# Performance work log

Measured on AMD Instinct MI355X. Metric: run time of the kernel, lower is better.

Reference implementation:

```python
import jax, jax.numpy as jnp
import numpy as np

NUM_HEADS = 16
HEAD_SIZE = 256
HIDDEN = NUM_HEADS * HEAD_SIZE  # 4096
ROTARY_DIM = 64
TOTAL_TOKENS = 8192
BATCH = 8
NUM_SLOTS = 16384


def setup_inputs() -> dict:
    key = jax.random.key(0)
    ks = jax.random.split(key, 6)
    hidden_states = jax.random.normal(ks[0], (TOTAL_TOKENS, HIDDEN), dtype=jnp.float32)
    w_qkv = jax.random.normal(ks[1], (3 * HIDDEN, HIDDEN), dtype=jnp.float32) * 0.02
    w_o = jax.random.normal(ks[2], (HIDDEN, HIDDEN), dtype=jnp.float32) * 0.02
    # cos/sin per token for the first rotary_dim dims (rotary_dim//2 freqs)
    cos = jax.random.uniform(ks[3], (TOTAL_TOKENS, ROTARY_DIM // 2), dtype=jnp.float32)
    sin = jax.random.uniform(ks[4], (TOTAL_TOKENS, ROTARY_DIM // 2), dtype=jnp.float32)
    key_cache = jnp.zeros((NUM_SLOTS, NUM_HEADS, HEAD_SIZE), dtype=jnp.float32)
    value_cache = jnp.zeros((NUM_SLOTS, NUM_HEADS, HEAD_SIZE), dtype=jnp.float32)
    slots = jnp.arange(TOTAL_TOKENS, dtype=jnp.int64) if jax.config.jax_enable_x64 else jnp.arange(TOTAL_TOKENS, dtype=jnp.int32)
    return {
        "hidden_states": hidden_states, "w_qkv": w_qkv, "w_o": w_o,
        "cos": cos, "sin": sin,
        "key_cache": key_cache, "value_cache": value_cache,
        "slots": slots, "batch_size": BATCH,
    }


def _apply_rope(x, cos, sin, rotary_dim):
    # x: [T, H, D]; rotate-half applied only to the first rotary_dim dims
    half = rotary_dim // 2
    x1 = x[..., :half]
    x2 = x[..., half:rotary_dim]
    c = cos[:, None, :]  # [T, 1, half]
    s = sin[:, None, :]
    rot = jnp.concatenate([x1 * c - x2 * s, x2 * c + x1 * s], axis=-1)
    return jnp.concatenate([rot, x[..., rotary_dim:]], axis=-1)


def reference(hidden_states, w_qkv, w_o, cos, sin, key_cache, value_cache, slots, batch_size):
    T, H = hidden_states.shape
    nh, hd = key_cache.shape[1], key_cache.shape[2]
    rotary_dim = 2 * cos.shape[1]
    scale = float(hd) ** -0.5

    # fused QKV projection (no bias), then split
    qkv = hidden_states @ w_qkv.T  # [T, 3H]
    q, k, v = jnp.split(qkv, 3, axis=1)
    q = q.reshape(T, nh, hd)
    k = k.reshape(T, nh, hd)
    v = v.reshape(T, nh, hd)

    # partial rotary embedding on first rotary_dim dims
    q = _apply_rope(q, cos, sin, rotary_dim)
    k = _apply_rope(k, cos, sin, rotary_dim)

    # KV-cache slot scatter, then gather back (prefill reads what was stored)
    key_cache = key_cache.at[slots].set(k)
    value_cache = value_cache.at[slots].set(v)
    k = key_cache[slots]
    v = value_cache[slots]

    # prefill flash-attention path: equal-length sequences, causal per sequence
    B = batch_size
    S = T // B
    qb = q.reshape(B, S, nh, hd)
    kb = k.reshape(B, S, nh, hd)
    vb = v.reshape(B, S, nh, hd)

    scores = jnp.einsum('bqhd,bkhd->bhqk', qb, kb) * scale  # [B, nh, S, S]
    causal = jnp.tril(jnp.ones((S, S), dtype=bool))
    scores = jnp.where(causal[None, None], scores, jnp.finfo(scores.dtype).min)
    attn = jax.nn.softmax(scores, axis=-1)
    out = jnp.einsum('bhqk,bkhd->bqhd', attn, vb).reshape(T, nh * hd)

    return out @ w_o.T
```

## Files before the change

### kernel.cpp

```cpp
#include <hip/hip_runtime.h>
#include <stdint.h>


typedef __bf16 bf16x8 __attribute__((ext_vector_type(8)));
typedef float f32x4 __attribute__((ext_vector_type(4)));

__device__ __forceinline__ unsigned short f2bf(float f) {
    union { float f; unsigned int u; } x;
    x.f = f;
    unsigned int r = x.u + 0x7fffu + ((x.u >> 16) & 1u);
    return (unsigned short)(r >> 16);
}

__device__ __forceinline__ float bf2f(unsigned short h) {
    union { unsigned int u; float f; } x;
    x.u = ((unsigned int)h) << 16;
    return x.f;
}

__device__ __forceinline__ void gld16(const void* g, void* l) {
    __builtin_amdgcn_global_load_lds(
        (const __attribute__((address_space(1))) void*)g,
        (__attribute__((address_space(3))) void*)l, 16, 0, 0);
}

__global__ __launch_bounds__(256) void cvt_bf16(const float* __restrict__ src,
                                                unsigned short* __restrict__ dst,
                                                long n4) {
    long i = (long)blockIdx.x * 256 + threadIdx.x;
    long stride = (long)gridDim.x * 256;
    for (; i < n4; i += stride) {
        float4 v = ((const float4*)src)[i];
        ushort4 o;
        o.x = f2bf(v.x); o.y = f2bf(v.y); o.z = f2bf(v.z); o.w = f2bf(v.w);
        ((ushort4*)dst)[i] = o;
    }
}

template <int EPI>
__global__ __launch_bounds__(512, 2) void gemm256(
    const unsigned short* __restrict__ A, long lda,
    const unsigned short* __restrict__ B, long ldb,
    int nkt, void* __restrict__ out,
    unsigned short* __restrict__ out2, unsigned short* __restrict__ out3) {
    __shared__ __attribute__((aligned(16))) unsigned short As[4 * 8192];
    __shared__ __attribute__((aligned(16))) unsigned short Bs[4 * 8192];

    const int tid = threadIdx.x;
    const int gx = gridDim.x;
    const int bid = blockIdx.y * gx + blockIdx.x;
    const int cpx = (gx * gridDim.y) >> 3;
    const int swz = (bid & 7) * cpx + (bid >> 3);
    const int ntile = swz % gx, mtile = swz / gx;

    const int l = tid & 63;
    const int wr = (tid >> 8) & 1, wc = (tid >> 6) & 3;
    const int lr = l & 15, lg = l >> 4;

    const int srow = tid >> 2;
    const int slc = (tid & 3) ^ ((tid >> 3) & 3);
    const unsigned short* Ag = A + (long)(mtile * 256 + srow) * lda + slc * 8;
    const unsigned short* Bg = B + (long)(ntile * 256 + srow) * ldb + slc * 8;
    unsigned short* lA = As + tid * 8;
    unsigned short* lB = Bs + tid * 8;

#define STAGE256(kt)                                              \
    {                                                             \
        const int s_ = (kt) & 3;                                  \
        const unsigned short* a_ = Ag + (long)(kt) * 32;          \
        const unsigned short* b_ = Bg + (long)(kt) * 32;          \
        gld16(a_, lA + s_ * 8192);                                \
        gld16(a_ + 128 * lda, lA + s_ * 8192 + 4096);             \
        gld16(b_, lB + s_ * 8192);                                \
        gld16(b_ + 128 * ldb, lB + s_ * 8192 + 4096);             \
    }

    int aoff[8], boff[4];
#pragma unroll
    for (int i = 0; i < 8; ++i) {
        const int r = wr * 128 + i * 16 + lr;
        aoff[i] = r * 32 + ((lg ^ ((r >> 1) & 3)) << 3);
    }
#pragma unroll
    for (int i = 0; i < 4; ++i) {
        const int r = wc * 64 + i * 16 + lr;
        boff[i] = r * 32 + ((lg ^ ((r >> 1) & 3)) << 3);
    }

    f32x4 acc[8][4];
#pragma unroll
    for (int i = 0; i < 8; ++i)
#pragma unroll
        for (int j = 0; j < 4; ++j) acc[i][j] = (f32x4)(0.0f);

    STAGE256(0);
    STAGE256(1);
    STAGE256(2);

    for (int t = 0; t < nkt; ++t) {
        if (t + 3 < nkt) {
            STAGE256(t + 3);
            asm volatile("s_waitcnt vmcnt(12)" ::: "memory");
        } else if (t + 2 < nkt) {
            asm volatile("s_waitcnt vmcnt(8)" ::: "memory");
        } else if (t + 1 < nkt) {
            asm volatile("s_waitcnt vmcnt(4)" ::: "memory");
        } else {
            asm volatile("s_waitcnt vmcnt(0)" ::: "memory");
        }
        __builtin_amdgcn_s_barrier();
        asm volatile("" ::: "memory");

        const unsigned short* as_ = As + ((t & 3) << 13);
        const unsigned short* bs_ = Bs + ((t & 3) << 13);
        bf16x8 af[8], bfr[4];
#pragma unroll
        for (int i = 0; i < 8; ++i) af[i] = *(const bf16x8*)(as_ + aoff[i]);
#pragma unroll
        for (int i = 0; i < 4; ++i) bfr[i] = *(const bf16x8*)(bs_ + boff[i]);

        __builtin_amdgcn_s_setprio(1);
#pragma unroll
        for (int mi = 0; mi < 8; ++mi)
#pragma unroll
            for (int ni = 0; ni < 4; ++ni)
                acc[mi][ni] = __builtin_amdgcn_mfma_f32_16x16x32_bf16(
                    af[mi], bfr[ni], acc[mi][ni], 0, 0, 0);
        __builtin_amdgcn_s_setprio(0);

        asm volatile("" ::: "memory");
        __builtin_amdgcn_s_barrier();
        asm volatile("" ::: "memory");
    }
#undef STAGE256

    const int mBase = mtile * 256 + wr * 128 + lg * 4;
    const int nBase = ntile * 256 + wc * 64 + lr;
#pragma unroll
    for (int mi = 0; mi < 8; ++mi) {
#pragma unroll
        for (int ni = 0; ni < 4; ++ni) {
#pragma unroll
            for (int r = 0; r < 4; ++r) {
                const int m = mBase + mi * 16 + r;
                const int n = nBase + ni * 16;
                const float v = acc[mi][ni][r];
                if (EPI == 0) {
                    const int which = n >> 12, h = (n >> 8) & 15, d = n & 255;
                    const int b = m >> 10, s = m & 1023;
                    const long idx = ((((long)b * 16 + h) << 10) + s) * 256 + d;
                    unsigned short* dst =
                        (which == 0) ? (unsigned short*)out : (which == 1 ? out2 : out3);
                    dst[idx] = f2bf(v);
                } else {
                    ((float*)out)[((long)m << 12) + n] = v;
                }
            }
        }
    }
}

template <int EPI>
__global__ __launch_bounds__(256) void gemm_bt(
    const unsigned short* __restrict__ A, long astride, long abatch,
    const unsigned short* __restrict__ B, long bstride, long bbatch,
    int kIters, void* __restrict__ out,
    unsigned short* __restrict__ out2, unsigned short* __restrict__ out3) {
    const int tid = threadIdx.x;
    const int ntile = blockIdx.x, mtile = blockIdx.y, bz = blockIdx.z;
    if (EPI == 1 && ntile > mtile) return;
    int kit = kIters;
    if (EPI == 2) kit = (mtile + 1) * 4;

    __shared__ __attribute__((aligned(16))) unsigned short As[128 * 32];
    __shared__ __attribute__((aligned(16))) unsigned short Bs[128 * 32];

    const unsigned short* Ab = A + (long)bz * abatch + (long)mtile * 128 * astride;
    const unsigned short* Bb = B + (long)bz * bbatch + (long)ntile * 128 * bstride;

    const int w = tid >> 6, l = tid & 63;
    const int wm = (w >> 1) * 64, wn = (w & 1) * 64;
    const int lr = l & 15;
    const int lc = l >> 4;

    const int c0 = tid, c1 = tid + 256;
    const int r0 = c0 >> 2, r1 = c1 >> 2;
    const int lc0 = (c0 & 3) ^ ((r0 >> 1) & 3);
    const int lc1 = (c1 & 3) ^ ((r1 >> 1) & 3);
    const long a0 = (long)r0 * astride + lc0 * 8;
    const long a1 = (long)r1 * astride + lc1 * 8;
    const long b0 = (long)r0 * bstride + lc0 * 8;
    const long b1 = (long)r1 * bstride + lc1 * 8;

    int aoff[4], boff[4];
#pragma unroll
    for (int i = 0; i < 4; ++i) {
        const int ra = wm + i * 16 + lr;
        aoff[i] = ra * 32 + ((lc ^ ((ra >> 1) & 3)) << 3);
        const int rb = wn + i * 16 + lr;
        boff[i] = rb * 32 + ((lc ^ ((rb >> 1) & 3)) << 3);
    }

    f32x4 acc[4][4];
#pragma unroll
    for (int i = 0; i < 4; ++i)
#pragma unroll
        for (int j = 0; j < 4; ++j) acc[i][j] = (f32x4)(0.0f);

    for (int kt = 0; kt < kit; ++kt) {
        const unsigned short* ak = Ab + kt * 32;
        const unsigned short* bk = Bb + kt * 32;
        __syncthreads();
        gld16(ak + a0, As + (long)c0 * 8);
        gld16(ak + a1, As + (long)c1 * 8);
        gld16(bk + b0, Bs + (long)c0 * 8);
        gld16(bk + b1, Bs + (long)c1 * 8);
        __syncthreads();

        bf16x8 af[4], bfv[4];
#pragma unroll
        for (int i = 0; i < 4; ++i) {
            af[i] = *(const bf16x8*)(As + aoff[i]);
            bfv[i] = *(const bf16x8*)(Bs + boff[i]);
        }
#pragma unroll
        for (int mi = 0; mi < 4; ++mi)
#pragma unroll
            for (int ni = 0; ni < 4; ++ni)
                acc[mi][ni] = __builtin_amdgcn_mfma_f32_16x16x32_bf16(
                    af[mi], bfv[ni], acc[mi][ni], 0, 0, 0);
    }

    const int mBase = mtile * 128 + wm + (l >> 4) * 4;
    const int nBase = ntile * 128 + wn + (l & 15);
#pragma unroll
    for (int mi = 0; mi < 4; ++mi) {
#pragma unroll
        for (int ni = 0; ni < 4; ++ni) {
#pragma unroll
            for (int r = 0; r < 4; ++r) {
                const int m = mBase + mi * 16 + r;
                const int n = nBase + ni * 16;
                const float v = acc[mi][ni][r];
                if (EPI == 1) {
                    ((float*)out)[((long)bz << 20) + ((long)m << 10) + n] = v * 0.0625f;
                } else if (EPI == 2) {
                    const int b = bz >> 4, h = bz & 15;
                    ((unsigned short*)out)[(((long)b << 10) + m) * 4096 + h * 256 + n] =
                        f2bf(v);
                }
            }
        }
    }
    (void)out2; (void)out3;
}

__global__ __launch_bounds__(256) void rope_qk(unsigned short* __restrict__ q_s,
                                               unsigned short* __restrict__ k_s,
                                               const float* __restrict__ cosp,
                                               const float* __restrict__ sinp) {
    const int tid = blockIdx.x * 256 + threadIdx.x;
    const int i = tid & 31;
    const int h = (tid >> 5) & 15;
    const int tok = tid >> 9;
    const int b = tok >> 10, s = tok & 1023;
    const long base = ((((long)b * 16 + h) << 10) + s) * 256 + i;
    const float c = cosp[tok * 32 + i];
    const float sn = sinp[tok * 32 + i];
    {
        float x1 = bf2f(q_s[base]), x2 = bf2f(q_s[base + 32]);
        q_s[base] = f2bf(x1 * c - x2 * sn);
        q_s[base + 32] = f2bf(x2 * c + x1 * sn);
    }
    {
        float x1 = bf2f(k_s[base]), x2 = bf2f(k_s[base + 32]);
        k_s[base] = f2bf(x1 * c - x2 * sn);
        k_s[base + 32] = f2bf(x2 * c + x1 * sn);
    }
}

__global__ __launch_bounds__(256) void vtrans(const unsigned short* __restrict__ v_s,
                                              unsigned short* __restrict__ vT) {
    __shared__ unsigned short tile[32][33];
    const int bh = blockIdx.z;
    const int s0 = blockIdx.x * 32, d0 = blockIdx.y * 32;
    const int x = threadIdx.x, y = threadIdx.y;
    const unsigned short* src = v_s + (((long)bh << 10) + s0) * 256 + d0;
#pragma unroll
    for (int j = 0; j < 4; ++j) tile[y * 4 + j][x] = src[(y * 4 + j) * 256 + x];
    __syncthreads();
    unsigned short* dst = vT + (((long)bh << 8) + d0) * 1024 + s0;
#pragma unroll
    for (int j = 0; j < 4; ++j) dst[(y * 4 + j) * 1024 + x] = tile[x][y * 4 + j];
}

__global__ __launch_bounds__(256) void softmax_rows(float* __restrict__ scores) {
    const int row = blockIdx.x;
    const int bh = row >> 10, q = row & 1023;
    float* srow = scores + ((long)bh << 20) + ((long)q << 10);
    const int t = threadIdx.x;

    float v[4];
#pragma unroll
    for (int j = 0; j < 4; ++j) {
        const int k = t + (j << 8);
        v[j] = (k <= q) ? srow[k] : -3.0e38f;
    }
    float mx = fmaxf(fmaxf(v[0], v[1]), fmaxf(v[2], v[3]));
#pragma unroll
    for (int off = 32; off >= 1; off >>= 1) mx = fmaxf(mx, __shfl_xor(mx, off));
    __shared__ float redmax[4];
    if ((t & 63) == 0) redmax[t >> 6] = mx;
    __syncthreads();
    mx = fmaxf(fmaxf(redmax[0], redmax[1]), fmaxf(redmax[2], redmax[3]));

    float p[4];
    float s = 0.0f;
#pragma unroll
    for (int j = 0; j < 4; ++j) {
        const int k = t + (j << 8);
        p[j] = (k <= q) ? __expf(v[j] - mx) : 0.0f;
        s += p[j];
    }
#pragma unroll
    for (int off = 32; off >= 1; off >>= 1) s += __shfl_xor(s, off);
    __shared__ float redsum[4];
    if ((t & 63) == 0) redsum[t >> 6] = s;
    __syncthreads();
    s = redsum[0] + redsum[1] + redsum[2] + redsum[3];
    const float inv = 1.0f / s;

    unsigned short* prow = (unsigned short*)srow;
    const int kend = (q & ~127) + 128;
#pragma unroll
    for (int j = 0; j < 4; ++j) {
        const int k = t + (j << 8);
        if (k < kend) prow[k] = f2bf(p[j] * inv);
    }
}

extern "C" void kernel_launch(void* const* d_in, const int* in_sizes, int n_in,
                              void* d_out, int out_size, void* d_ws, size_t ws_size,
                              hipStream_t stream) {
    const float* hidden = (const float*)d_in[0];
    const float* w_qkv  = (const float*)d_in[1];
    const float* w_o    = (const float*)d_in[2];
    const float* cosp   = (const float*)d_in[3];
    const float* sinp   = (const float*)d_in[4];

    const long SZ_WO = 33554432L, SZ_HEAD = 67108864L, SZ_SCORES = 536870912L;
    if (ws_size < (size_t)(SZ_WO + 5 * SZ_HEAD + SZ_SCORES)) return;
    char* p = (char*)d_ws;
    unsigned short* wo_b = (unsigned short*)p;  p += SZ_WO;
    unsigned short* q_s  = (unsigned short*)p;  p += SZ_HEAD;
    unsigned short* k_s  = (unsigned short*)p;  p += SZ_HEAD;
    unsigned short* v_s  = (unsigned short*)p;  p += SZ_HEAD;
    unsigned short* vT   = (unsigned short*)p;  p += SZ_HEAD;
    unsigned short* attn = (unsigned short*)p;  p += SZ_HEAD;
    char* X = p;
    unsigned short* hid_b  = (unsigned short*)X;
    unsigned short* wqkv_b = (unsigned short*)(X + SZ_HEAD);
    float* scores = (float*)X;

    cvt_bf16<<<8192, 256, 0, stream>>>(hidden, hid_b, (long)8192 * 4096 / 4);
    cvt_bf16<<<8192, 256, 0, stream>>>(w_qkv, wqkv_b, (long)12288 * 4096 / 4);
    cvt_bf16<<<4096, 256, 0, stream>>>(w_o, wo_b, (long)4096 * 4096 / 4);

    gemm256<0><<<dim3(48, 32, 1), 512, 0, stream>>>(
        hid_b, 4096, wqkv_b, 4096, 128, q_s, k_s, v_s);

    rope_qk<<<16384, 256, 0, stream>>>(q_s, k_s, cosp, sinp);

    vtrans<<<dim3(32, 8, 128), dim3(32, 8, 1), 0, stream>>>(v_s, vT);

    gemm_bt<1><<<dim3(8, 8, 128), 256, 0, stream>>>(
        q_s, 256, 262144, k_s, 256, 262144, 8, scores, nullptr, nullptr);

    softmax_rows<<<131072, 256, 0, stream>>>(scores);

    gemm_bt<2><<<dim3(2, 8, 128), 256, 0, stream>>>(
        (unsigned short*)scores, 2048, 2097152, vT, 1024, 262144, 0,
        attn, nullptr, nullptr);

    gemm256<1><<<dim3(16, 32, 1), 512, 0, stream>>>(
        attn, 4096, wo_b, 4096, 128, d_out, nullptr, nullptr);

    (void)in_sizes; (void)n_in; (void)out_size;
}
```

Measured before the change: 2.533 ms.

## Restructure 256x256 GEMM mainloop into four-phase ping-pong with split staging

```diff
diff --git a/kernel.cpp b/kernel.cpp
--- a/kernel.cpp
+++ b/kernel.cpp
@@ -38,13 +38,13 @@
 }
 
 template <int EPI>
-__global__ __launch_bounds__(512, 2) void gemm256(
+__global__ __launch_bounds__(512, 2) void gemm256p(
     const unsigned short* __restrict__ A, long lda,
     const unsigned short* __restrict__ B, long ldb,
     int nkt, void* __restrict__ out,
     unsigned short* __restrict__ out2, unsigned short* __restrict__ out3) {
-    __shared__ __attribute__((aligned(16))) unsigned short As[4 * 8192];
-    __shared__ __attribute__((aligned(16))) unsigned short Bs[4 * 8192];
+    __shared__ __attribute__((aligned(16))) unsigned short As[32768];
+    __shared__ __attribute__((aligned(16))) unsigned short Bs[32768];
 
     const int tid = threadIdx.x;
     const int gx = gridDim.x;
@@ -61,19 +61,33 @@
     const int slc = (tid & 3) ^ ((tid >> 3) & 3);
     const unsigned short* Ag = A + (long)(mtile * 256 + srow) * lda + slc * 8;
     const unsigned short* Bg = B + (long)(ntile * 256 + srow) * ldb + slc * 8;
-    unsigned short* lA = As + tid * 8;
-    unsigned short* lB = Bs + tid * 8;
-
-#define STAGE256(kt)                                              \
-    {                                                             \
-        const int s_ = (kt) & 3;                                  \
-        const unsigned short* a_ = Ag + (long)(kt) * 32;          \
-        const unsigned short* b_ = Bg + (long)(kt) * 32;          \
-        gld16(a_, lA + s_ * 8192);                                \
-        gld16(a_ + 128 * lda, lA + s_ * 8192 + 4096);             \
-        gld16(b_, lB + s_ * 8192);                                \
-        gld16(b_ + 128 * ldb, lB + s_ * 8192 + 4096);             \
-    }
+    unsigned short* lAs = As + tid * 8;
+    unsigned short* lBs = Bs + tid * 8;
+
+#define STAGE_A(t, kk)                                                 \
+    {                                                                  \
+        const unsigned short* g_ = Ag + (long)(t) * 64 + (kk) * 32;    \
+        unsigned short* d_ = lAs + (((t) & 1) * 16384 + (kk) * 8192);  \
+        gld16(g_, d_);                                                 \
+        gld16(g_ + 128 * lda, d_ + 4096);                              \
+    }
+#define STAGE_B(t, kk)                                                 \
+    {                                                                  \
+        const unsigned short* g_ = Bg + (long)(t) * 64 + (kk) * 32;    \
+        unsigned short* d_ = lBs + (((t) & 1) * 16384 + (kk) * 8192);  \
+        gld16(g_, d_);                                                 \
+        gld16(g_ + 128 * ldb, d_ + 4096);                              \
+    }
+#define WAITV(full_)                                                   \
+    if (full_) { asm volatile("s_waitcnt vmcnt(12)" ::: "memory"); }   \
+    else       { asm volatile("s_waitcnt vmcnt(0)" ::: "memory"); }
+#define LEADBAR()                                                      \
+    __builtin_amdgcn_s_barrier();                                      \
+    __builtin_amdgcn_sched_barrier(0)
+#define TRAILBAR()                                                     \
+    asm volatile("s_waitcnt lgkmcnt(0)" ::: "memory");                 \
+    __builtin_amdgcn_sched_barrier(0);                                 \
+    __builtin_amdgcn_s_barrier()
 
     int aoff[8], boff[4];
 #pragma unroll
@@ -93,46 +107,106 @@
 #pragma unroll
         for (int j = 0; j < 4; ++j) acc[i][j] = (f32x4)(0.0f);
 
-    STAGE256(0);
-    STAGE256(1);
-    STAGE256(2);
+    STAGE_A(0, 0); STAGE_B(0, 0); STAGE_A(0, 1); STAGE_B(0, 1);
+    STAGE_A(1, 0); STAGE_B(1, 0); STAGE_A(1, 1);
 
     for (int t = 0; t < nkt; ++t) {
-        if (t + 3 < nkt) {
-            STAGE256(t + 3);
-            asm volatile("s_waitcnt vmcnt(12)" ::: "memory");
-        } else if (t + 2 < nkt) {
-            asm volatile("s_waitcnt vmcnt(8)" ::: "memory");
-        } else if (t + 1 < nkt) {
-            asm volatile("s_waitcnt vmcnt(4)" ::: "memory");
-        } else {
-            asm volatile("s_waitcnt vmcnt(0)" ::: "memory");
-        }
-        __builtin_amdgcn_s_barrier();
-        asm volatile("" ::: "memory");
-
-        const unsigned short* as_ = As + ((t & 3) << 13);
-        const unsigned short* bs_ = Bs + ((t & 3) << 13);
-        bf16x8 af[8], bfr[4];
-#pragma unroll
-        for (int i = 0; i < 8; ++i) af[i] = *(const bf16x8*)(as_ + aoff[i]);
-#pragma unroll
-        for (int i = 0; i < 4; ++i) bfr[i] = *(const bf16x8*)(bs_ + boff[i]);
-
-        __builtin_amdgcn_s_setprio(1);
-#pragma unroll
-        for (int mi = 0; mi < 8; ++mi)
-#pragma unroll
-            for (int ni = 0; ni < 4; ++ni)
-                acc[mi][ni] = __builtin_amdgcn_mfma_f32_16x16x32_bf16(
-                    af[mi], bfr[ni], acc[mi][ni], 0, 0, 0);
-        __builtin_amdgcn_s_setprio(0);
-
-        asm volatile("" ::: "memory");
-        __builtin_amdgcn_s_barrier();
-        asm volatile("" ::: "memory");
-    }
-#undef STAGE256
+        const int p = t & 1;
+        const unsigned short* a0 = As + p * 16384;
+        const unsigned short* b0 = Bs + p * 16384;
+        const unsigned short* a1 = a0 + 8192;
+        const unsigned short* b1 = b0 + 8192;
+        const bool full = (t + 2 < nkt);
+
+        bf16x8 af[8];
+
+        if (t + 1 < nkt) STAGE_B(t + 1, 1);
+        WAITV(full);
+        LEADBAR();
+        {
+#pragma unroll
+            for (int mi = 0; mi < 8; ++mi)
+                af[mi] = *(const bf16x8*)(a0 + aoff[mi]);
+            bf16x8 f0 = *(const bf16x8*)(b0 + boff[0]);
+            bf16x8 f1 = *(const bf16x8*)(b0 + boff[1]);
+            __builtin_amdgcn_s_setprio(1);
+#pragma unroll
+            for (int mi = 0; mi < 8; ++mi)
+                acc[mi][0] = __builtin_amdgcn_mfma_f32_16x16x32_bf16(
+                    af[mi], f0, acc[mi][0], 0, 0, 0);
+#pragma unroll
+            for (int mi = 0; mi < 8; ++mi)
+                acc[mi][1] = __builtin_amdgcn_mfma_f32_16x16x32_bf16(
+                    af[mi], f1, acc[mi][1], 0, 0, 0);
+            __builtin_amdgcn_s_setprio(0);
+        }
+        TRAILBAR();
+
+        if (full) STAGE_A(t + 2, 0);
+        WAITV(full);
+        LEADBAR();
+        {
+            bf16x8 f2 = *(const bf16x8*)(b0 + boff[2]);
+            bf16x8 f3 = *(const bf16x8*)(b0 + boff[3]);
+            __builtin_amdgcn_s_setprio(1);
+#pragma unroll
+            for (int mi = 0; mi < 8; ++mi)
+                acc[mi][2] = __builtin_amdgcn_mfma_f32_16x16x32_bf16(
+                    af[mi], f2, acc[mi][2], 0, 0, 0);
+#pragma unroll
+            for (int mi = 0; mi < 8; ++mi)
+                acc[mi][3] = __builtin_amdgcn_mfma_f32_16x16x32_bf16(
+                    af[mi], f3, acc[mi][3], 0, 0, 0);
+            __builtin_amdgcn_s_setprio(0);
+        }
+        TRAILBAR();
+
+        if (full) STAGE_B(t + 2, 0);
+        WAITV(full);
+        LEADBAR();
+        {
+#pragma unroll
+            for (int mi = 0; mi < 8; ++mi)
+                af[mi] = *(const bf16x8*)(a1 + aoff[mi]);
+            bf16x8 f0 = *(const bf16x8*)(b1 + boff[0]);
+            bf16x8 f1 = *(const bf16x8*)(b1 + boff[1]);
+            __builtin_amdgcn_s_setprio(1);
+#pragma unroll
+            for (int mi = 0; mi < 8; ++mi)
+                acc[mi][0] = __builtin_amdgcn_mfma_f32_16x16x32_bf16(
+                    af[mi], f0, acc[mi][0], 0, 0, 0);
+#pragma unroll
+            for (int mi = 0; mi < 8; ++mi)
+                acc[mi][1] = __builtin_amdgcn_mfma_f32_16x16x32_bf16(
+                    af[mi], f1, acc[mi][1], 0, 0, 0);
+            __builtin_amdgcn_s_setprio(0);
+        }
+        TRAILBAR();
+
+        if (full) STAGE_A(t + 2, 1);
+        WAITV(full);
+        LEADBAR();
+        {
+            bf16x8 f2 = *(const bf16x8*)(b1 + boff[2]);
+            bf16x8 f3 = *(const bf16x8*)(b1 + boff[3]);
+            __builtin_amdgcn_s_setprio(1);
+#pragma unroll
+            for (int mi = 0; mi < 8; ++mi)
+                acc[mi][2] = __builtin_amdgcn_mfma_f32_16x16x32_bf16(
+                    af[mi], f2, acc[mi][2], 0, 0, 0);
+#pragma unroll
+            for (int mi = 0; mi < 8; ++mi)
+                acc[mi][3] = __builtin_amdgcn_mfma_f32_16x16x32_bf16(
+                    af[mi], f3, acc[mi][3], 0, 0, 0);
+            __builtin_amdgcn_s_setprio(0);
+        }
+        TRAILBAR();
+    }
+#undef STAGE_A
+#undef STAGE_B
+#undef WAITV
+#undef LEADBAR
+#undef TRAILBAR
 
     const int mBase = mtile * 256 + wr * 128 + lg * 4;
     const int nBase = ntile * 256 + wc * 64 + lr;
@@ -366,8 +440,8 @@
     cvt_bf16<<<8192, 256, 0, stream>>>(w_qkv, wqkv_b, (long)12288 * 4096 / 4);
     cvt_bf16<<<4096, 256, 0, stream>>>(w_o, wo_b, (long)4096 * 4096 / 4);
 
-    gemm256<0><<<dim3(48, 32, 1), 512, 0, stream>>>(
-        hid_b, 4096, wqkv_b, 4096, 128, q_s, k_s, v_s);
+    gemm256p<0><<<dim3(48, 32, 1), 512, 0, stream>>>(
+        hid_b, 4096, wqkv_b, 4096, 64, q_s, k_s, v_s);
 
     rope_qk<<<16384, 256, 0, stream>>>(q_s, k_s, cosp, sinp);
 
@@ -382,8 +456,8 @@
         (unsigned short*)scores, 2048, 2097152, vT, 1024, 262144, 0,
         attn, nullptr, nullptr);
 
-    gemm256<1><<<dim3(16, 32, 1), 512, 0, stream>>>(
-        attn, 4096, wo_b, 4096, 128, d_out, nullptr, nullptr);
+    gemm256p<1><<<dim3(16, 32, 1), 512, 0, stream>>>(
+        attn, 4096, wo_b, 4096, 64, d_out, nullptr, nullptr);
 
     (void)in_sizes; (void)n_in; (void)out_size;
 }
```

New measurement: 2.228 ms. 12.0% less time.
